# Kernel tuning notes

Measured on AMD Instinct MI355X. Metric: run time of the kernel, lower is better.

Reference implementation:

```python
import jax, jax.numpy as jnp
import numpy as np

# SMPL kinematic tree parents (joint 0 is root)
SMPL_PARENTS = [-1, 0, 0, 0, 1, 2, 3, 4, 5, 6, 7, 8, 9, 9, 9, 12, 13, 14, 16, 17, 18, 19, 20, 21]
NUM_JOINTS = 24


def _rodrigues(axisang):
    # axisang: (B, J, 3) -> (B, J, 3, 3), matching th_posemap_axisang's eps handling
    angle = jnp.linalg.norm(axisang + 1e-8, axis=-1, keepdims=True)  # (B,J,1)
    axis = axisang / angle
    a = angle[..., None]                      # (B,J,1,1)
    c, s = jnp.cos(a), jnp.sin(a)
    x, y, z = axis[..., 0], axis[..., 1], axis[..., 2]
    zero = jnp.zeros_like(x)
    # skew-symmetric cross-product matrix K
    K = jnp.stack([
        jnp.stack([zero, -z, y], axis=-1),
        jnp.stack([z, zero, -x], axis=-1),
        jnp.stack([-y, x, zero], axis=-1),
    ], axis=-2)                               # (B,J,3,3)
    outer = axis[..., :, None] * axis[..., None, :]
    eye = jnp.eye(3, dtype=axisang.dtype)
    return c * eye + (1.0 - c) * outer + s * K


def setup_inputs() -> dict:
    key = jax.random.key(0)
    k1, k2, k3 = jax.random.split(key, 3)
    B, N = 16, 100000
    normals = jax.random.normal(k1, (B, 3, N), dtype=jnp.float32)
    pose = jax.random.normal(k2, (B, 72), dtype=jnp.float32)
    skinning_weights = jax.random.uniform(k3, (B, NUM_JOINTS, N), dtype=jnp.float32)
    return {"normals": normals, "pose": pose, "skinning_weights": skinning_weights}


def reference(normals, pose, skinning_weights):
    B = pose.shape[0]
    rots = _rodrigues(pose.reshape(B, NUM_JOINTS, 3))  # (B,24,3,3)
    # sequential kinematic-chain composition over the fixed 24-joint tree
    results = [rots[:, 0]]
    for i in range(1, NUM_JOINTS):
        results.append(jnp.matmul(results[SMPL_PARENTS[i]], rots[:, i]))
    th_results2 = jnp.stack(results, axis=-1)          # (B,3,3,24)
    # skinning: (B,9,24) @ (B,24,N) -> (B,3,3,N)
    n_T = jnp.einsum('bijk,bkn->bijn', th_results2, skinning_weights)
    # rotate normals: sum over local axis j of n_T[b,i,j,n] * normals[b,j,n]
    n_verts = jnp.einsum('bijn,bjn->bin', n_T, normals)  # (B,3,N)
    return n_verts
```

## Files before the change

### kernel.cpp

```cpp
#include <hip/hip_runtime.h>

#define NUM_JOINTS 24

typedef float fvec4 __attribute__((ext_vector_type(4)));

__device__ __constant__ int d_chain[NUM_JOINTS][9] = {
    {0,-1,-1,-1,-1,-1,-1,-1,-1},
    {0,1,-1,-1,-1,-1,-1,-1,-1},
    {0,2,-1,-1,-1,-1,-1,-1,-1},
    {0,3,-1,-1,-1,-1,-1,-1,-1},
    {0,1,4,-1,-1,-1,-1,-1,-1},
    {0,2,5,-1,-1,-1,-1,-1,-1},
    {0,3,6,-1,-1,-1,-1,-1,-1},
    {0,1,4,7,-1,-1,-1,-1,-1},
    {0,2,5,8,-1,-1,-1,-1,-1},
    {0,3,6,9,-1,-1,-1,-1,-1},
    {0,1,4,7,10,-1,-1,-1,-1},
    {0,2,5,8,11,-1,-1,-1,-1},
    {0,3,6,9,12,-1,-1,-1,-1},
    {0,3,6,9,13,-1,-1,-1,-1},
    {0,3,6,9,14,-1,-1,-1,-1},
    {0,3,6,9,12,15,-1,-1,-1},
    {0,3,6,9,13,16,-1,-1,-1},
    {0,3,6,9,14,17,-1,-1,-1},
    {0,3,6,9,13,16,18,-1,-1},
    {0,3,6,9,14,17,19,-1,-1},
    {0,3,6,9,13,16,18,20,-1},
    {0,3,6,9,14,17,19,21,-1},
    {0,3,6,9,13,16,18,20,22},
    {0,3,6,9,14,17,19,21,23},
};

__device__ __forceinline__ fvec4 fma4s(fvec4 a, float s, fvec4 c) {
    fvec4 r;
    r.x = fmaf(a.x, s, c.x); r.y = fmaf(a.y, s, c.y);
    r.z = fmaf(a.z, s, c.z); r.w = fmaf(a.w, s, c.w);
    return r;
}
__device__ __forceinline__ fvec4 fma4v(fvec4 a, fvec4 b, fvec4 c) {
    fvec4 r;
    r.x = fmaf(a.x, b.x, c.x); r.y = fmaf(a.y, b.y, c.y);
    r.z = fmaf(a.z, b.z, c.z); r.w = fmaf(a.w, b.w, c.w);
    return r;
}
__device__ __forceinline__ fvec4 mul4s(fvec4 a, float s) {
    fvec4 r; r.x = a.x * s; r.y = a.y * s; r.z = a.z * s; r.w = a.w * s;
    return r;
}

__global__ __launch_bounds__(256) void skin_fused16_kernel(
    const float* __restrict__ normals,
    const float* __restrict__ pose,
    const float* __restrict__ weights,
    float* __restrict__ out,
    int N) {
    __shared__ float L[NUM_JOINTS][9];
    __shared__ fvec4 Rl[NUM_JOINTS][3];

    const int b = blockIdx.y;
    const int tid = threadIdx.x;

    if (tid < NUM_JOINTS) {
        float x = pose[b * 72 + tid * 3 + 0];
        float y = pose[b * 72 + tid * 3 + 1];
        float z = pose[b * 72 + tid * 3 + 2];
        float ax = x + 1e-8f, ay = y + 1e-8f, az = z + 1e-8f;
        float angle = sqrtf(ax * ax + ay * ay + az * az);
        float inv = 1.0f / angle;
        float ux = x * inv, uy = y * inv, uz = z * inv;
        float c = __cosf(angle), s = __sinf(angle), t = 1.0f - c;
        L[tid][0] = c + t * ux * ux;
        L[tid][1] = t * ux * uy - s * uz;
        L[tid][2] = t * ux * uz + s * uy;
        L[tid][3] = t * uy * ux + s * uz;
        L[tid][4] = c + t * uy * uy;
        L[tid][5] = t * uy * uz - s * ux;
        L[tid][6] = t * uz * ux - s * uy;
        L[tid][7] = t * uz * uy + s * ux;
        L[tid][8] = c + t * uz * uz;
    }
    __syncthreads();

    if (tid < NUM_JOINTS) {
        float G[9];
        int j0 = d_chain[tid][0];
        #pragma unroll
        for (int e = 0; e < 9; e++) G[e] = L[j0][e];
        #pragma unroll
        for (int d = 1; d < 9; d++) {
            int j = d_chain[tid][d];
            if (j >= 0) {
                float T[9];
                #pragma unroll
                for (int r = 0; r < 3; r++) {
                    #pragma unroll
                    for (int cc = 0; cc < 3; cc++) {
                        T[r * 3 + cc] = G[r * 3 + 0] * L[j][0 * 3 + cc]
                                      + G[r * 3 + 1] * L[j][1 * 3 + cc]
                                      + G[r * 3 + 2] * L[j][2 * 3 + cc];
                    }
                }
                #pragma unroll
                for (int e = 0; e < 9; e++) G[e] = T[e];
            }
        }
        float* Rf = (float*)Rl;
        #pragma unroll
        for (int e = 0; e < 9; e++) Rf[tid * 12 + e] = G[e];
    }
    __syncthreads();

    const int q = blockIdx.x * blockDim.x + tid;
    const int nf4 = N >> 2;
    const int n16 = nf4 >> 2;

    const fvec4* __restrict__ Wb = (const fvec4*)(weights + (size_t)b * NUM_JOINTS * N);
    const fvec4* __restrict__ Nb = (const fvec4*)(normals + (size_t)b * 3 * N);
    fvec4* __restrict__ Ob = (fvec4*)(out + (size_t)b * 3 * N);

    if (q < n16) {
        int qg[4];
        #pragma unroll
        for (int g = 0; g < 4; g++) qg[g] = q + g * n16;

        fvec4 nx[4], ny[4], nz[4], o0[4], o1[4], o2[4];
        #pragma unroll
        for (int g = 0; g < 4; g++) {
            nx[g] = __builtin_nontemporal_load(&Nb[(size_t)0 * nf4 + qg[g]]);
            ny[g] = __builtin_nontemporal_load(&Nb[(size_t)1 * nf4 + qg[g]]);
            nz[g] = __builtin_nontemporal_load(&Nb[(size_t)2 * nf4 + qg[g]]);
            o0[g] = (fvec4)(0.f); o1[g] = (fvec4)(0.f); o2[g] = (fvec4)(0.f);
        }

        #pragma unroll 2
        for (int k = 0; k < NUM_JOINTS; k++) {
            fvec4 w[4];
            #pragma unroll
            for (int g = 0; g < 4; g++)
                w[g] = __builtin_nontemporal_load(&Wb[(size_t)k * nf4 + qg[g]]);
            fvec4 r0 = Rl[k][0];
            fvec4 r1 = Rl[k][1];
            fvec4 r2 = Rl[k][2];
            #pragma unroll
            for (int g = 0; g < 4; g++) {
                fvec4 t0 = fma4s(nx[g], r0.x, fma4s(ny[g], r0.y, mul4s(nz[g], r0.z)));
                fvec4 t1 = fma4s(nx[g], r0.w, fma4s(ny[g], r1.x, mul4s(nz[g], r1.y)));
                fvec4 t2 = fma4s(nx[g], r1.z, fma4s(ny[g], r1.w, mul4s(nz[g], r2.x)));
                o0[g] = fma4v(w[g], t0, o0[g]);
                o1[g] = fma4v(w[g], t1, o1[g]);
                o2[g] = fma4v(w[g], t2, o2[g]);
            }
        }

        #pragma unroll
        for (int g = 0; g < 4; g++) {
            __builtin_nontemporal_store(o0[g], &Ob[(size_t)0 * nf4 + qg[g]]);
            __builtin_nontemporal_store(o1[g], &Ob[(size_t)1 * nf4 + qg[g]]);
            __builtin_nontemporal_store(o2[g], &Ob[(size_t)2 * nf4 + qg[g]]);
        }
    } else if (q == n16) {
        const float* Rf = (const float*)Rl;
        for (int n = n16 * 16; n < N; n++) {
            float vx = normals[(size_t)b * 3 * N + 0 * N + n];
            float vy = normals[(size_t)b * 3 * N + 1 * N + n];
            float vz = normals[(size_t)b * 3 * N + 2 * N + n];
            float s0 = 0.f, s1 = 0.f, s2 = 0.f;
            for (int k = 0; k < NUM_JOINTS; k++) {
                float w = weights[(size_t)b * NUM_JOINTS * N + (size_t)k * N + n];
                float t0 = Rf[k*12+0] * vx + Rf[k*12+1] * vy + Rf[k*12+2] * vz;
                float t1 = Rf[k*12+3] * vx + Rf[k*12+4] * vy + Rf[k*12+5] * vz;
                float t2 = Rf[k*12+6] * vx + Rf[k*12+7] * vy + Rf[k*12+8] * vz;
                s0 = fmaf(w, t0, s0); s1 = fmaf(w, t1, s1); s2 = fmaf(w, t2, s2);
            }
            out[(size_t)b * 3 * N + 0 * N + n] = s0;
            out[(size_t)b * 3 * N + 1 * N + n] = s1;
            out[(size_t)b * 3 * N + 2 * N + n] = s2;
        }
    }
}

extern "C" void kernel_launch(void* const* d_in, const int* in_sizes, int n_in,
                              void* d_out, int out_size, void* d_ws, size_t ws_size,
                              hipStream_t stream) {
    const float* normals = (const float*)d_in[0];
    const float* pose = (const float*)d_in[1];
    const float* weights = (const float*)d_in[2];
    float* out = (float*)d_out;

    const int B = in_sizes[1] / 72;
    const int N = in_sizes[0] / (3 * B);

    const int n16 = (N >> 2) >> 2;
    const int slots = n16 + 1;
    const int gx = (slots + 255) / 256;
    skin_fused16_kernel<<<dim3(gx, B), dim3(256), 0, stream>>>(normals, pose, weights, out, N);
}
```

Before: 224.9 us.

## Process one float4 per thread with an 8-deep rolling weight prefetch

Each thread now handles a single float4 of vertices instead of four, so the grid is four times larger. A ring of eight register-held weight loads is issued ahead of use across the fully unrolled 24-joint loop. The aim is more waves in flight and more outstanding loads to hide memory latency in this bandwidth-bound kernel. The cost is that the per-block preamble (Rodrigues plus chain composition) is repeated across four times as many blocks, and there is less memory-level parallelism per thread.

```diff
diff --git a/kernel.cpp b/kernel.cpp
--- a/kernel.cpp
+++ b/kernel.cpp
@@ -48,7 +48,9 @@
     return r;
 }
 
-__global__ __launch_bounds__(256) void skin_fused16_kernel(
+#define PF 8
+
+__global__ __launch_bounds__(256) void skin_fused4_kernel(
     const float* __restrict__ normals,
     const float* __restrict__ pose,
     const float* __restrict__ weights,
@@ -112,55 +114,46 @@
 
     const int q = blockIdx.x * blockDim.x + tid;
     const int nf4 = N >> 2;
-    const int n16 = nf4 >> 2;
 
     const fvec4* __restrict__ Wb = (const fvec4*)(weights + (size_t)b * NUM_JOINTS * N);
     const fvec4* __restrict__ Nb = (const fvec4*)(normals + (size_t)b * 3 * N);
     fvec4* __restrict__ Ob = (fvec4*)(out + (size_t)b * 3 * N);
 
-    if (q < n16) {
-        int qg[4];
+    if (q < nf4) {
+        fvec4 nx = __builtin_nontemporal_load(&Nb[(size_t)0 * nf4 + q]);
+        fvec4 ny = __builtin_nontemporal_load(&Nb[(size_t)1 * nf4 + q]);
+        fvec4 nz = __builtin_nontemporal_load(&Nb[(size_t)2 * nf4 + q]);
+
+        fvec4 w[PF];
         #pragma unroll
-        for (int g = 0; g < 4; g++) qg[g] = q + g * n16;
+        for (int j = 0; j < PF; j++)
+            w[j] = __builtin_nontemporal_load(&Wb[(size_t)j * nf4 + q]);
 
-        fvec4 nx[4], ny[4], nz[4], o0[4], o1[4], o2[4];
+        fvec4 o0 = (fvec4)(0.f), o1 = (fvec4)(0.f), o2 = (fvec4)(0.f);
+
         #pragma unroll
-        for (int g = 0; g < 4; g++) {
-            nx[g] = __builtin_nontemporal_load(&Nb[(size_t)0 * nf4 + qg[g]]);
-            ny[g] = __builtin_nontemporal_load(&Nb[(size_t)1 * nf4 + qg[g]]);
-            nz[g] = __builtin_nontemporal_load(&Nb[(size_t)2 * nf4 + qg[g]]);
-            o0[g] = (fvec4)(0.f); o1[g] = (fvec4)(0.f); o2[g] = (fvec4)(0.f);
-        }
-
-        #pragma unroll 2
         for (int k = 0; k < NUM_JOINTS; k++) {
-            fvec4 w[4];
-            #pragma unroll
-            for (int g = 0; g < 4; g++)
-                w[g] = __builtin_nontemporal_load(&Wb[(size_t)k * nf4 + qg[g]]);
+            fvec4 wk = w[k & (PF - 1)];
+            if (k + PF < NUM_JOINTS)
+                w[k & (PF - 1)] =
+                    __builtin_nontemporal_load(&Wb[(size_t)(k + PF) * nf4 + q]);
             fvec4 r0 = Rl[k][0];
             fvec4 r1 = Rl[k][1];
             fvec4 r2 = Rl[k][2];
-            #pragma unroll
-            for (int g = 0; g < 4; g++) {
-                fvec4 t0 = fma4s(nx[g], r0.x, fma4s(ny[g], r0.y, mul4s(nz[g], r0.z)));
-                fvec4 t1 = fma4s(nx[g], r0.w, fma4s(ny[g], r1.x, mul4s(nz[g], r1.y)));
-                fvec4 t2 = fma4s(nx[g], r1.z, fma4s(ny[g], r1.w, mul4s(nz[g], r2.x)));
-                o0[g] = fma4v(w[g], t0, o0[g]);
-                o1[g] = fma4v(w[g], t1, o1[g]);
-                o2[g] = fma4v(w[g], t2, o2[g]);
-            }
+            fvec4 t0 = fma4s(nx, r0.x, fma4s(ny, r0.y, mul4s(nz, r0.z)));
+            fvec4 t1 = fma4s(nx, r0.w, fma4s(ny, r1.x, mul4s(nz, r1.y)));
+            fvec4 t2 = fma4s(nx, r1.z, fma4s(ny, r1.w, mul4s(nz, r2.x)));
+            o0 = fma4v(wk, t0, o0);
+            o1 = fma4v(wk, t1, o1);
+            o2 = fma4v(wk, t2, o2);
         }
 
-        #pragma unroll
-        for (int g = 0; g < 4; g++) {
-            __builtin_nontemporal_store(o0[g], &Ob[(size_t)0 * nf4 + qg[g]]);
-            __builtin_nontemporal_store(o1[g], &Ob[(size_t)1 * nf4 + qg[g]]);
-            __builtin_nontemporal_store(o2[g], &Ob[(size_t)2 * nf4 + qg[g]]);
-        }
-    } else if (q == n16) {
+        __builtin_nontemporal_store(o0, &Ob[(size_t)0 * nf4 + q]);
+        __builtin_nontemporal_store(o1, &Ob[(size_t)1 * nf4 + q]);
+        __builtin_nontemporal_store(o2, &Ob[(size_t)2 * nf4 + q]);
+    } else if (q == nf4) {
         const float* Rf = (const float*)Rl;
-        for (int n = n16 * 16; n < N; n++) {
+        for (int n = nf4 * 4; n < N; n++) {
             float vx = normals[(size_t)b * 3 * N + 0 * N + n];
             float vy = normals[(size_t)b * 3 * N + 1 * N + n];
             float vz = normals[(size_t)b * 3 * N + 2 * N + n];
@@ -190,8 +183,8 @@
     const int B = in_sizes[1] / 72;
     const int N = in_sizes[0] / (3 * B);
 
-    const int n16 = (N >> 2) >> 2;
-    const int slots = n16 + 1;
+    const int nf4 = N >> 2;
+    const int slots = nf4 + 1;
     const int gx = (slots + 255) / 256;
-    skin_fused16_kernel<<<dim3(gx, B), dim3(256), 0, stream>>>(normals, pose, weights, out, N);
+    skin_fused4_kernel<<<dim3(gx, B), dim3(256), 0, stream>>>(normals, pose, weights, out, N);
 }
```

Result: slower. 250.0 us (+11.2%).
